# Optimization experiments

Hardware: AMD Instinct MI355X
Metric: run time of the kernel (lower is better)

Reference implementation:

```python
import jax, jax.numpy as jnp
import numpy as np

N_NODES = 10000
N_EDGES = 160000
DIM = 512
LN_EPS = 1e-5


def setup_inputs() -> dict:
    key = jax.random.key(0)
    ks = jax.random.split(key, 6)
    scale = 1.0 / np.sqrt(DIM)
    h = jax.random.normal(ks[0], (N_NODES, DIM), dtype=jnp.float32)
    edge_index = jax.random.randint(ks[1], (2, N_EDGES), 0, N_NODES, dtype=jnp.int32)
    W_self = jax.random.normal(ks[2], (DIM, DIM), dtype=jnp.float32) * scale
    b_self = jnp.zeros((DIM,), dtype=jnp.float32)
    W_neigh = jax.random.normal(ks[3], (DIM, DIM), dtype=jnp.float32) * scale
    b_neigh = jnp.zeros((DIM,), dtype=jnp.float32)
    ln_gamma = jnp.ones((DIM,), dtype=jnp.float32)
    ln_beta = jnp.zeros((DIM,), dtype=jnp.float32)
    return {"h": h, "edge_index": edge_index, "W_self": W_self, "b_self": b_self,
            "W_neigh": W_neigh, "b_neigh": b_neigh, "ln_gamma": ln_gamma, "ln_beta": ln_beta}


def reference(h, edge_index, W_self, b_self, W_neigh, b_neigh, ln_gamma, ln_beta):
    n = h.shape[0]
    src = edge_index[0]
    dst = edge_index[1]
    # per-edge message: gather dst features, dense linear (torch Linear => x @ W.T + b)
    msg = h[dst] @ W_neigh.T + b_neigh            # [E, dim]
    # scatter-add aggregate into src nodes
    neigh = jax.ops.segment_sum(msg, src, num_segments=n)            # [N, dim]
    deg = jax.ops.segment_sum(jnp.ones(src.shape, h.dtype), src, num_segments=n)
    deg = jnp.maximum(deg, 1.0)
    neigh = neigh / deg[:, None]
    # self transform + relu (dropout is identity in eval)
    out = jax.nn.relu(h @ W_self.T + b_self + neigh)
    # residual LayerNorm
    x = h + out
    mean = jnp.mean(x, axis=-1, keepdims=True)
    var = jnp.mean(jnp.square(x - mean), axis=-1, keepdims=True)
    return (x - mean) * jax.lax.rsqrt(var + LN_EPS) * ln_gamma + ln_beta
```

## Files before the change

kernel.cpp:

```cpp
#include <hip/hip_runtime.h>

#define N_NODES 10000
#define N_PAD   10048
#define N_EDGES 160000
#define DIM     512
#define KDIM    1024
#define CAP     64

#define BM 64
#define BN 128
#define BK 64
#define KITERS (KDIM / BK)
#define NWG    ((N_PAD / BM) * (DIM / BN))
#define SWZ_Q  (NWG / 8)
#define SWZ_R  (NWG % 8)

typedef __attribute__((ext_vector_type(8))) short bf16x8;
typedef __attribute__((ext_vector_type(4))) float f32x4;
typedef __attribute__((ext_vector_type(2))) float f32x2;

static __device__ __forceinline__ ushort f2bf(float f) {
    union { float f; unsigned u; } x; x.f = f;
    unsigned u = x.u + 0x7fff + ((x.u >> 16) & 1);
    return (ushort)(u >> 16);
}
static __device__ __forceinline__ float b2f(ushort u) {
    union { unsigned u; float f; } x; x.u = ((unsigned)u) << 16; return x.f;
}

__global__ __launch_bounds__(256) void conv_all(
    const float* __restrict__ Wself, const float* __restrict__ Wneigh,
    ushort* __restrict__ Wc,
    const float* __restrict__ h, ushort* __restrict__ X,
    unsigned char* __restrict__ H8,
    const int* __restrict__ eidx, int* __restrict__ cnt, int* __restrict__ col)
{
    int idx = blockIdx.x * 256 + threadIdx.x;

    if (idx < DIM * 128) {
        int c  = idx >> 7;
        int k8 = idx & 127;
        const float* src = (k8 < 64) ? (Wself + (size_t)c * DIM + k8 * 8)
                                     : (Wneigh + (size_t)c * DIM + (k8 - 64) * 8);
        float4 v0 = *(const float4*)src;
        float4 v1 = *(const float4*)(src + 4);
        ushort* dst = Wc + (size_t)c * KDIM + k8 * 8;
        ushort4 o0 = { f2bf(v0.x), f2bf(v0.y), f2bf(v0.z), f2bf(v0.w) };
        ushort4 o1 = { f2bf(v1.x), f2bf(v1.y), f2bf(v1.z), f2bf(v1.w) };
        *(ushort4*)dst = o0;
        *(ushort4*)(dst + 4) = o1;
    }

    if (idx < N_EDGES) {
        int s = eidx[idx];
        int d = eidx[N_EDGES + idx];
        int p = atomicAdd(&cnt[s], 1);
        if (p < CAP) col[(s << 6) + p] = d;
    }

    int n  = idx >> 7;
    int k8 = idx & 127;
    if (n >= N_PAD) return;
    ushort* dst = X + (size_t)n * KDIM + k8 * 8;
    if (n >= N_NODES) {
        ushort4 z = {0, 0, 0, 0};
        *(ushort4*)dst = z;
        *(ushort4*)(dst + 4) = z;
        return;
    }
    if (k8 >= 64) return;
    const float* src = h + (size_t)n * DIM + k8 * 8;
    float4 v0 = *(const float4*)src;
    float4 v1 = *(const float4*)(src + 4);
    ushort4 o0 = { f2bf(v0.x), f2bf(v0.y), f2bf(v0.z), f2bf(v0.w) };
    ushort4 o1 = { f2bf(v1.x), f2bf(v1.y), f2bf(v1.z), f2bf(v1.w) };
    *(ushort4*)dst = o0;
    *(ushort4*)(dst + 4) = o1;
    uint2 p8;
    int r0 = 0, r1 = 0;
    r0 = __builtin_amdgcn_cvt_pk_fp8_f32(v0.x, v0.y, r0, false);
    r0 = __builtin_amdgcn_cvt_pk_fp8_f32(v0.z, v0.w, r0, true);
    r1 = __builtin_amdgcn_cvt_pk_fp8_f32(v1.x, v1.y, r1, false);
    r1 = __builtin_amdgcn_cvt_pk_fp8_f32(v1.z, v1.w, r1, true);
    p8.x = (unsigned)r0;
    p8.y = (unsigned)r1;
    *(uint2*)(H8 + (size_t)n * DIM + k8 * 8) = p8;
}

__global__ __launch_bounds__(256) void gather_agg(
    const int* __restrict__ cnt, const int* __restrict__ col,
    const unsigned char* __restrict__ H8,
    ushort* __restrict__ X, float* __restrict__ deg)
{
    int gid  = blockIdx.x * 256 + threadIdx.x;
    int n    = gid >> 6;
    int lane = gid & 63;
    if (n >= N_NODES) return;
    int d  = cnt[n];
    int nk = d < CAP ? d : CAP;

    int myc = (lane < nk) ? col[(n << 6) + lane] : 0;

    f32x2 a01 = {0.f, 0.f}, a23 = {0.f, 0.f}, a45 = {0.f, 0.f}, a67 = {0.f, 0.f};
    int k = 0;
    for (; k + 8 <= nk; k += 8) {
        uint2 v[8];
#pragma unroll
        for (int u = 0; u < 8; ++u) {
            int dst = __shfl(myc, k + u);
            v[u] = *(const uint2*)(H8 + (size_t)dst * DIM + lane * 8);
        }
#pragma unroll
        for (int u = 0; u < 8; ++u) {
            a01 += __builtin_amdgcn_cvt_pk_f32_fp8((int)v[u].x, false);
            a23 += __builtin_amdgcn_cvt_pk_f32_fp8((int)v[u].x, true);
            a45 += __builtin_amdgcn_cvt_pk_f32_fp8((int)v[u].y, false);
            a67 += __builtin_amdgcn_cvt_pk_f32_fp8((int)v[u].y, true);
        }
    }
    for (; k < nk; ++k) {
        int dst = __shfl(myc, k);
        uint2 v = *(const uint2*)(H8 + (size_t)dst * DIM + lane * 8);
        a01 += __builtin_amdgcn_cvt_pk_f32_fp8((int)v.x, false);
        a23 += __builtin_amdgcn_cvt_pk_f32_fp8((int)v.x, true);
        a45 += __builtin_amdgcn_cvt_pk_f32_fp8((int)v.y, false);
        a67 += __builtin_amdgcn_cvt_pk_f32_fp8((int)v.y, true);
    }
    float inv = 1.0f / fmaxf((float)d, 1.0f);
    ushort* xr = X + (size_t)n * KDIM + DIM + lane * 8;
    ushort4 o0 = { f2bf(a01[0] * inv), f2bf(a01[1] * inv),
                   f2bf(a23[0] * inv), f2bf(a23[1] * inv) };
    ushort4 o1 = { f2bf(a45[0] * inv), f2bf(a45[1] * inv),
                   f2bf(a67[0] * inv), f2bf(a67[1] * inv) };
    *(ushort4*)xr       = o0;
    *(ushort4*)(xr + 4) = o1;
    if (lane == 0) deg[n] = (float)d;
}

#define MFMA(A, B, C) __builtin_amdgcn_mfma_f32_16x16x32_bf16(A, B, C, 0, 0, 0)

__global__ __launch_bounds__(256) void mfma_gemm(
    const ushort* __restrict__ X, const ushort* __restrict__ Wc,
    const float* __restrict__ deg,
    const float* __restrict__ bself, const float* __restrict__ bneigh,
    ushort* __restrict__ Y)
{
    __shared__ ushort As[2][BM * BK];
    __shared__ ushort Bs[2][BN * BK];

    const int orig = blockIdx.x;
    const int xcd  = orig & 7;
    const int loc  = orig >> 3;
    const int wgid = (xcd < SWZ_R ? xcd * (SWZ_Q + 1)
                                  : SWZ_R * (SWZ_Q + 1) + (xcd - SWZ_R) * SWZ_Q) + loc;
    const int row0 = (wgid >> 2) * BM;
    const int col0 = (wgid & 3) * BN;

    const int t    = threadIdx.x;
    const int lane = t & 63;
    const int wave = t >> 6;
    const int wr   = (wave >> 1) * 32;
    const int wc   = (wave & 1) * 64;
    const int fr   = lane & 15;
    const int fq   = lane >> 4;

#define STAGE(BUF, IT)                                                         \
    {                                                                          \
        const int k0s = (IT) * BK;                                             \
        _Pragma("unroll")                                                      \
        for (int s = 0; s < 2; ++s) {                                          \
            int c = t + s * 256;                                               \
            int row = c >> 3;                                                  \
            int ks = k0s + (((c & 7) ^ (row & 7)) << 3);                       \
            __builtin_amdgcn_global_load_lds(                                  \
                (const __attribute__((address_space(1))) void*)                \
                    (X + (size_t)(row0 + row) * KDIM + ks),                    \
                (__attribute__((address_space(3))) void*)(&As[BUF][c * 8]),    \
                16, 0, 0);                                                     \
        }                                                                      \
        _Pragma("unroll")                                                      \
        for (int s = 0; s < 4; ++s) {                                          \
            int c = t + s * 256;                                               \
            int row = c >> 3;                                                  \
            int ks = k0s + (((c & 7) ^ (row & 7)) << 3);                       \
            __builtin_amdgcn_global_load_lds(                                  \
                (const __attribute__((address_space(1))) void*)                \
                    (Wc + (size_t)(col0 + row) * KDIM + ks),                   \
                (__attribute__((address_space(3))) void*)(&Bs[BUF][c * 8]),    \
                16, 0, 0);                                                     \
        }                                                                      \
    }

    f32x4 acc[2][4];
#pragma unroll
    for (int i = 0; i < 2; ++i)
#pragma unroll
        for (int j = 0; j < 4; ++j) acc[i][j] = (f32x4){0.f, 0.f, 0.f, 0.f};

    STAGE(0, 0);
    __syncthreads();

    int buf = 0;
    for (int it = 0; it < KITERS; ++it) {
        if (it + 1 < KITERS) STAGE(buf ^ 1, it + 1);

        const ushort* as = As[buf];
        const ushort* bs = Bs[buf];
#pragma unroll
        for (int inner = 0; inner < 2; ++inner) {
            const int sw = (((inner * 4 + fq) ^ (fr & 7)) << 3);
            bf16x8 a0 = *(const bf16x8*)(as + (wr + fr) * BK + sw);
            bf16x8 a1 = *(const bf16x8*)(as + (wr + 16 + fr) * BK + sw);
#pragma unroll
            for (int j = 0; j < 4; ++j) {
                bf16x8 bv = *(const bf16x8*)(bs + (wc + j * 16 + fr) * BK + sw);
                acc[0][j] = MFMA(a0, bv, acc[0][j]);
                acc[1][j] = MFMA(a1, bv, acc[1][j]);
            }
        }
        __syncthreads();
        buf ^= 1;
    }

#pragma unroll
    for (int i = 0; i < 2; ++i) {
#pragma unroll
        for (int r = 0; r < 4; ++r) {
            int gr = row0 + wr + i * 16 + fq * 4 + r;
            float hb = (gr < N_NODES && deg[gr] > 0.0f) ? 1.0f : 0.0f;
            ushort* yrow = Y + (size_t)gr * DIM;
#pragma unroll
            for (int j = 0; j < 4; ++j) {
                int gc = col0 + wc + j * 16 + fr;
                float v = fmaxf(acc[i][j][r] + bself[gc] + hb * bneigh[gc], 0.f);
                yrow[gc] = f2bf(v);
            }
        }
    }
}

__global__ __launch_bounds__(512) void ln_kernel(
    const ushort* __restrict__ Y, const ushort* __restrict__ Xl,
    const float* __restrict__ g, const float* __restrict__ b,
    float* __restrict__ out)
{
    __shared__ float red[2][8];
    const int half = threadIdx.x >> 8;
    const int t    = threadIdx.x & 255;
    const int n    = blockIdx.x * 2 + half;

    ushort2 yv = *(const ushort2*)(Y  + (size_t)n * DIM  + t * 2);
    ushort2 xv = *(const ushort2*)(Xl + (size_t)n * KDIM + t * 2);
    float v0 = b2f(xv.x) + b2f(yv.x);
    float v1 = b2f(xv.y) + b2f(yv.y);
    float s  = v0 + v1;
    float sq = v0 * v0 + v1 * v1;
#pragma unroll
    for (int off = 32; off >= 1; off >>= 1) {
        s  += __shfl_xor(s, off);
        sq += __shfl_xor(sq, off);
    }
    int wave = t >> 6;
    if ((t & 63) == 0) { red[half][wave] = s; red[half][4 + wave] = sq; }
    __syncthreads();
    s  = red[half][0] + red[half][1] + red[half][2] + red[half][3];
    sq = red[half][4] + red[half][5] + red[half][6] + red[half][7];
    float mean = s * (1.0f / DIM);
    float var  = sq * (1.0f / DIM) - mean * mean;
    float rstd = rsqrtf(var + 1e-5f);
    float2 gv = *(const float2*)(g + t * 2);
    float2 bv = *(const float2*)(b + t * 2);
    float2 o;
    o.x = (v0 - mean) * rstd * gv.x + bv.x;
    o.y = (v1 - mean) * rstd * gv.y + bv.y;
    *(float2*)(out + (size_t)n * DIM + t * 2) = o;
}

extern "C" void kernel_launch(void* const* d_in, const int* in_sizes, int n_in,
                              void* d_out, int out_size, void* d_ws, size_t ws_size,
                              hipStream_t stream)
{
    const float* h      = (const float*)d_in[0];
    const int*   eidx   = (const int*)d_in[1];
    const float* Wself  = (const float*)d_in[2];
    const float* bself  = (const float*)d_in[3];
    const float* Wneigh = (const float*)d_in[4];
    const float* bneigh = (const float*)d_in[5];
    const float* gamma  = (const float*)d_in[6];
    const float* beta   = (const float*)d_in[7];
    float* out = (float*)d_out;

    ushort* X   = (ushort*)d_ws;
    ushort* Wc  = X + (size_t)N_PAD * KDIM;
    ushort* Y   = Wc + (size_t)DIM * KDIM;
    float* deg  = (float*)(Y + (size_t)N_PAD * DIM);
    int* cnt    = (int*)(deg + N_NODES);
    int* col    = cnt + N_NODES;
    unsigned char* H8 = (unsigned char*)(col + (size_t)N_NODES * CAP);

    hipMemsetAsync(cnt, 0, N_NODES * sizeof(int), stream);

    conv_all<<<(N_PAD * 128) / 256, 256, 0, stream>>>(
        Wself, Wneigh, Wc, h, X, H8, eidx, cnt, col);

    gather_agg<<<(N_NODES * 64) / 256, 256, 0, stream>>>(cnt, col, H8, X, deg);

    mfma_gemm<<<NWG, 256, 0, stream>>>(X, Wc, deg, bself, bneigh, Y);

    ln_kernel<<<N_NODES / 2, 512, 0, stream>>>(Y, X, gamma, beta, out);
}
```

Measured before the change: 71.04 us.

## Split GEMM K dimension in two and fuse bias/ReLU into LayerNorm

The fused self/neighbor GEMM is split along K into two halves, which doubles the number of workgroups and halves BK to 32. Each half writes its own bf16 partial output. The bias, degree mask and ReLU epilogue move into the LayerNorm kernel, which now sums the two partials. The aim is better CU occupancy and load balance for the GEMM, at the cost of an extra Y buffer write/read and the bf16 rounding of each partial before summation.

Result: faster. 68.82 us (median of 2 runs) (-3.1%).

```diff
diff --git a/kernel.cpp b/kernel.cpp
--- a/kernel.cpp
+++ b/kernel.cpp
@@ -9,9 +9,9 @@
 
 #define BM 64
 #define BN 128
-#define BK 64
-#define KITERS (KDIM / BK)
-#define NWG    ((N_PAD / BM) * (DIM / BN))
+#define BK 32
+#define KITERS (DIM / BK)
+#define NWG    ((N_PAD / BM) * (DIM / BN) * 2)
 #define SWZ_Q  (NWG / 8)
 #define SWZ_R  (NWG % 8)
 
@@ -141,20 +141,16 @@
 
 __global__ __launch_bounds__(256) void mfma_gemm(
     const ushort* __restrict__ X, const ushort* __restrict__ Wc,
-    const float* __restrict__ deg,
-    const float* __restrict__ bself, const float* __restrict__ bneigh,
     ushort* __restrict__ Y)
 {
     __shared__ ushort As[2][BM * BK];
     __shared__ ushort Bs[2][BN * BK];
 
     const int orig = blockIdx.x;
-    const int xcd  = orig & 7;
-    const int loc  = orig >> 3;
-    const int wgid = (xcd < SWZ_R ? xcd * (SWZ_Q + 1)
-                                  : SWZ_R * (SWZ_Q + 1) + (xcd - SWZ_R) * SWZ_Q) + loc;
-    const int row0 = (wgid >> 2) * BM;
-    const int col0 = (wgid & 3) * BN;
+    const int wgid = (orig & 7) * SWZ_Q + (orig >> 3);
+    const int kb   = wgid & 1;
+    const int col0 = ((wgid >> 1) & 3) * BN;
+    const int row0 = (wgid >> 3) * BM;
 
     const int t    = threadIdx.x;
     const int lane = t & 63;
@@ -166,23 +162,21 @@
 
 #define STAGE(BUF, IT)                                                         \
     {                                                                          \
-        const int k0s = (IT) * BK;                                             \
+        const int k0s = kb * DIM + (IT) * BK;                                  \
+        {                                                                      \
+            int row = t >> 2;                                                  \
+            int ks = k0s + (((t & 3) ^ (row & 3)) << 3);                       \
+            __builtin_amdgcn_global_load_lds(                                  \
+                (const __attribute__((address_space(1))) void*)                \
+                    (X + (size_t)(row0 + row) * KDIM + ks),                    \
+                (__attribute__((address_space(3))) void*)(&As[BUF][t * 8]),    \
+                16, 0, 0);                                                     \
+        }                                                                      \
         _Pragma("unroll")                                                      \
         for (int s = 0; s < 2; ++s) {                                          \
             int c = t + s * 256;                                               \
-            int row = c >> 3;                                                  \
-            int ks = k0s + (((c & 7) ^ (row & 7)) << 3);                       \
-            __builtin_amdgcn_global_load_lds(                                  \
-                (const __attribute__((address_space(1))) void*)                \
-                    (X + (size_t)(row0 + row) * KDIM + ks),                    \
-                (__attribute__((address_space(3))) void*)(&As[BUF][c * 8]),    \
-                16, 0, 0);                                                     \
-        }                                                                      \
-        _Pragma("unroll")                                                      \
-        for (int s = 0; s < 4; ++s) {                                          \
-            int c = t + s * 256;                                               \
-            int row = c >> 3;                                                  \
-            int ks = k0s + (((c & 7) ^ (row & 7)) << 3);                       \
+            int row = c >> 2;                                                  \
+            int ks = k0s + (((c & 3) ^ (row & 3)) << 3);                       \
             __builtin_amdgcn_global_load_lds(                                  \
                 (const __attribute__((address_space(1))) void*)                \
                     (Wc + (size_t)(col0 + row) * KDIM + ks),                   \
@@ -206,34 +200,30 @@
 
         const ushort* as = As[buf];
         const ushort* bs = Bs[buf];
-#pragma unroll
-        for (int inner = 0; inner < 2; ++inner) {
-            const int sw = (((inner * 4 + fq) ^ (fr & 7)) << 3);
-            bf16x8 a0 = *(const bf16x8*)(as + (wr + fr) * BK + sw);
-            bf16x8 a1 = *(const bf16x8*)(as + (wr + 16 + fr) * BK + sw);
-#pragma unroll
-            for (int j = 0; j < 4; ++j) {
-                bf16x8 bv = *(const bf16x8*)(bs + (wc + j * 16 + fr) * BK + sw);
-                acc[0][j] = MFMA(a0, bv, acc[0][j]);
-                acc[1][j] = MFMA(a1, bv, acc[1][j]);
-            }
+        const int sw = ((fq ^ (fr & 3)) << 3);
+        bf16x8 a0 = *(const bf16x8*)(as + (wr + fr) * BK + sw);
+        bf16x8 a1 = *(const bf16x8*)(as + (wr + 16 + fr) * BK + sw);
+#pragma unroll
+        for (int j = 0; j < 4; ++j) {
+            bf16x8 bv = *(const bf16x8*)(bs + (wc + j * 16 + fr) * BK + sw);
+            acc[0][j] = MFMA(a0, bv, acc[0][j]);
+            acc[1][j] = MFMA(a1, bv, acc[1][j]);
         }
         __syncthreads();
         buf ^= 1;
     }
 
+    ushort* Yk = Y + (size_t)kb * N_PAD * DIM;
 #pragma unroll
     for (int i = 0; i < 2; ++i) {
 #pragma unroll
         for (int r = 0; r < 4; ++r) {
             int gr = row0 + wr + i * 16 + fq * 4 + r;
-            float hb = (gr < N_NODES && deg[gr] > 0.0f) ? 1.0f : 0.0f;
-            ushort* yrow = Y + (size_t)gr * DIM;
+            ushort* yrow = Yk + (size_t)gr * DIM;
 #pragma unroll
             for (int j = 0; j < 4; ++j) {
                 int gc = col0 + wc + j * 16 + fr;
-                float v = fmaxf(acc[i][j][r] + bself[gc] + hb * bneigh[gc], 0.f);
-                yrow[gc] = f2bf(v);
+                yrow[gc] = f2bf(acc[i][j][r]);
             }
         }
     }
@@ -241,6 +231,8 @@
 
 __global__ __launch_bounds__(512) void ln_kernel(
     const ushort* __restrict__ Y, const ushort* __restrict__ Xl,
+    const float* __restrict__ deg,
+    const float* __restrict__ bself, const float* __restrict__ bneigh,
     const float* __restrict__ g, const float* __restrict__ b,
     float* __restrict__ out)
 {
@@ -249,10 +241,14 @@
     const int t    = threadIdx.x & 255;
     const int n    = blockIdx.x * 2 + half;
 
-    ushort2 yv = *(const ushort2*)(Y  + (size_t)n * DIM  + t * 2);
+    float hb = (deg[n] > 0.0f) ? 1.0f : 0.0f;
+    ushort2 y0 = *(const ushort2*)(Y + (size_t)n * DIM + t * 2);
+    ushort2 y1 = *(const ushort2*)(Y + (size_t)(N_PAD + n) * DIM + t * 2);
     ushort2 xv = *(const ushort2*)(Xl + (size_t)n * KDIM + t * 2);
-    float v0 = b2f(xv.x) + b2f(yv.x);
-    float v1 = b2f(xv.y) + b2f(yv.y);
+    float2 bsv = *(const float2*)(bself + t * 2);
+    float2 bnv = *(const float2*)(bneigh + t * 2);
+    float v0 = b2f(xv.x) + fmaxf(b2f(y0.x) + b2f(y1.x) + bsv.x + hb * bnv.x, 0.f);
+    float v1 = b2f(xv.y) + fmaxf(b2f(y0.y) + b2f(y1.y) + bsv.y + hb * bnv.y, 0.f);
     float s  = v0 + v1;
     float sq = v0 * v0 + v1 * v1;
 #pragma unroll
@@ -293,7 +289,7 @@
     ushort* X   = (ushort*)d_ws;
     ushort* Wc  = X + (size_t)N_PAD * KDIM;
     ushort* Y   = Wc + (size_t)DIM * KDIM;
-    float* deg  = (float*)(Y + (size_t)N_PAD * DIM);
+    float* deg  = (float*)(Y + (size_t)2 * N_PAD * DIM);
     int* cnt    = (int*)(deg + N_NODES);
     int* col    = cnt + N_NODES;
     unsigned char* H8 = (unsigned char*)(col + (size_t)N_NODES * CAP);
@@ -305,7 +301,8 @@
 
     gather_agg<<<(N_NODES * 64) / 256, 256, 0, stream>>>(cnt, col, H8, X, deg);
 
-    mfma_gemm<<<NWG, 256, 0, stream>>>(X, Wc, deg, bself, bneigh, Y);
-
-    ln_kernel<<<N_NODES / 2, 512, 0, stream>>>(Y, X, gamma, beta, out);
-}
+    mfma_gemm<<<NWG, 256, 0, stream>>>(X, Wc, Y);
+
+    ln_kernel<<<N_NODES / 2, 512, 0, stream>>>(Y, X, deg, bself, bneigh,
+                                               gamma, beta, out);
+}
```
